# Kernel tuning notes

Hardware: AMD Instinct MI355X
Metric: run time of the kernel (lower is better)

## Reference

```python
import jax, jax.numpy as jnp
import numpy as np

N_NODES = 100000
N_EDGES = 1600000
D_FEAT = 256
HIDDEN = 256
N_CLASSES = 64


def gcn_conv(x, edge_index, W, b, num_nodes):
    """PyG GCNConv: h = W x; add self loops; symmetric D^-1/2 (A+I) D^-1/2 aggregation; + bias."""
    h = x @ W  # [N, out]
    loop = jnp.arange(num_nodes, dtype=edge_index.dtype)
    row = jnp.concatenate([edge_index[0], loop])  # source nodes
    col = jnp.concatenate([edge_index[1], loop])  # target nodes
    deg = jax.ops.segment_sum(jnp.ones_like(col, dtype=h.dtype), col, num_segments=num_nodes)
    dinv = jnp.where(deg > 0, jax.lax.rsqrt(deg), 0.0)
    norm = dinv[row] * dinv[col]  # per-edge normalization
    out = jax.ops.segment_sum(h[row] * norm[:, None], col, num_segments=num_nodes)
    return out + b


def setup_inputs() -> dict:
    key = jax.random.key(0)
    k1, k2, k3, k4 = jax.random.split(key, 4)
    x = jax.random.normal(k1, (N_NODES, D_FEAT), dtype=jnp.float32)
    edge_index = jax.random.randint(k2, (2, N_EDGES), 0, N_NODES, dtype=jnp.int64)
    W1 = jax.random.normal(k3, (D_FEAT, HIDDEN), dtype=jnp.float32) * (1.0 / np.sqrt(D_FEAT))
    b1 = jnp.zeros((HIDDEN,), dtype=jnp.float32)
    W2 = jax.random.normal(k4, (HIDDEN, N_CLASSES), dtype=jnp.float32) * (1.0 / np.sqrt(HIDDEN))
    b2 = jnp.zeros((N_CLASSES,), dtype=jnp.float32)
    return {"x": x, "edge_index": edge_index, "W1": W1, "b1": b1, "W2": W2, "b2": b2}


def reference(x, edge_index, W1, b1, W2, b2):
    # conv1 -> relu -> dropout (eval mode: identity) -> conv2
    h = gcn_conv(x, edge_index, W1, b1, N_NODES)
    h = jax.nn.relu(h)
    out = gcn_conv(h, edge_index, W2, b2, N_NODES)  # [N, num_classes]
    return out
```

## Files before the change

### kernel.cpp

```cpp
#include <hip/hip_runtime.h>
#include <hip/hip_bf16.h>

#define N_NODES 100000
#define N_EDGES 1600000
#define D_FEAT 256
#define HIDDEN 256
#define N_CLASSES 64

#define NBKT 391
#define TILE 4096
#define CAP  8192
#define RB_TOT 6256

typedef __attribute__((ext_vector_type(8))) short bf16x8;
typedef __attribute__((ext_vector_type(4))) float f32x4;

__device__ inline float b2f(ushort u) {
    unsigned v = ((unsigned)u) << 16;
    float f; __builtin_memcpy(&f, &v, 4); return f;
}
__device__ inline ushort f2b(float f) {
    unsigned u; __builtin_memcpy(&u, &f, 4);
    unsigned r = (u + 0x7fffu + ((u >> 16) & 1u)) >> 16;
    return (ushort)r;
}

__global__ __launch_bounds__(256)
void zero_bcnt(int* bcnt) {
    int i = blockIdx.x * 256 + threadIdx.x;
    if (i < NBKT) bcnt[i] = 0;
}

__global__ __launch_bounds__(256)
void bin_count(const int* __restrict__ cols, int* bcnt, int nE) {
    __shared__ int h[NBKT];
    int t = threadIdx.x;
    for (int i = t; i < NBKT; i += 256) h[i] = 0;
    __syncthreads();
    for (long e = (long)blockIdx.x * 256 + t; e < nE; e += (long)gridDim.x * 256)
        atomicAdd(&h[cols[e] >> 8], 1);
    __syncthreads();
    for (int i = t; i < NBKT; i += 256)
        if (h[i]) atomicAdd(&bcnt[i], h[i]);
}

__global__ __launch_bounds__(256)
void bucket_scan(const int* __restrict__ bcnt, int* __restrict__ bbase,
                 int* __restrict__ bcur, int* __restrict__ offsets) {
    __shared__ int sd[256];
    int t = threadIdx.x;
    int i0 = 2 * t, i1 = 2 * t + 1;
    int a = (i0 < NBKT) ? bcnt[i0] : 0;
    int b = (i1 < NBKT) ? bcnt[i1] : 0;
    int s = a + b;
    sd[t] = s; __syncthreads();
    #pragma unroll
    for (int off = 1; off < 256; off <<= 1) {
        int v = (t >= off) ? sd[t - off] : 0;
        __syncthreads();
        sd[t] += v;
        __syncthreads();
    }
    int ex = sd[t] - s;
    if (i0 <= NBKT) bbase[i0] = ex;
    if (i0 < NBKT)  bcur[i0] = ex;
    if (i1 <= NBKT) bbase[i1] = ex + a;
    if (i1 < NBKT)  bcur[i1] = ex + a;
    if (t == 0) offsets[N_NODES] = N_EDGES;
}

__global__ __launch_bounds__(256)
void bin_scatter(const int* __restrict__ rows, const int* __restrict__ cols,
                 int* bcur, unsigned* __restrict__ bins, int nE)
{
    __shared__ unsigned recs[TILE];
    __shared__ ushort bos[TILE];
    __shared__ int hist[NBKT], excl[NBKT], cursor[NBKT], gbase[NBKT];
    __shared__ int sd[256];
    int t = threadIdx.x;
    long e0 = (long)blockIdx.x * TILE;
    int cnt = (int)min((long)TILE, (long)nE - e0);
    for (int i = t; i < NBKT; i += 256) hist[i] = 0;
    __syncthreads();
    int myrow[TILE / 256], mycol[TILE / 256];
    #pragma unroll
    for (int k = 0; k < TILE / 256; ++k) {
        int i = k * 256 + t;
        if (i < cnt) {
            myrow[k] = rows[e0 + i];
            mycol[k] = cols[e0 + i];
            atomicAdd(&hist[mycol[k] >> 8], 1);
        }
    }
    __syncthreads();
    {
        int i0 = 2 * t, i1 = 2 * t + 1;
        int a = (i0 < NBKT) ? hist[i0] : 0;
        int b = (i1 < NBKT) ? hist[i1] : 0;
        int s = a + b;
        sd[t] = s; __syncthreads();
        #pragma unroll
        for (int off = 1; off < 256; off <<= 1) {
            int v = (t >= off) ? sd[t - off] : 0;
            __syncthreads();
            sd[t] += v;
            __syncthreads();
        }
        int ex = sd[t] - s;
        if (i0 < NBKT) { excl[i0] = ex;     cursor[i0] = ex; }
        if (i1 < NBKT) { excl[i1] = ex + a; cursor[i1] = ex + a; }
    }
    __syncthreads();
    #pragma unroll
    for (int k = 0; k < TILE / 256; ++k) {
        int i = k * 256 + t;
        if (i < cnt) {
            int b = mycol[k] >> 8;
            int s = atomicAdd(&cursor[b], 1);
            recs[s] = ((unsigned)(mycol[k] & 255) << 24) | (unsigned)myrow[k];
            bos[s] = (ushort)b;
        }
    }
    __syncthreads();
    for (int i = t; i < NBKT; i += 256)
        if (hist[i] > 0) gbase[i] = atomicAdd(&bcur[i], hist[i]);
    __syncthreads();
    for (int i = t; i < cnt; i += 256) {
        int b = bos[i];
        bins[gbase[b] + (i - excl[b])] = recs[i];
    }
}

__global__ __launch_bounds__(256)
void bucket_fill(const unsigned* __restrict__ bins, const int* __restrict__ bbase,
                 int* __restrict__ offsets, float* __restrict__ dinv,
                 int* __restrict__ esrc)
{
    int b = blockIdx.x, t = threadIdx.x;
    int s0 = bbase[b], s1 = bbase[b + 1];
    int len = s1 - s0;
    __shared__ int cnt[256];
    __shared__ int sd[256];
    __shared__ int cur[256];
    __shared__ int stage[CAP];
    cnt[t] = 0;
    __syncthreads();
    for (int i = t; i < len; i += 256) atomicAdd(&cnt[bins[s0 + i] >> 24], 1);
    __syncthreads();
    int c = cnt[t];
    sd[t] = c; __syncthreads();
    #pragma unroll
    for (int off = 1; off < 256; off <<= 1) {
        int v = (t >= off) ? sd[t - off] : 0;
        __syncthreads();
        sd[t] += v;
        __syncthreads();
    }
    int ex = sd[t] - c;
    cur[t] = ex;
    int node = b * 256 + t;
    if (node < N_NODES) {
        offsets[node] = s0 + ex;
        dinv[node] = rsqrtf(1.0f + (float)c);
    }
    __syncthreads();
    if (len <= CAP) {
        for (int i = t; i < len; i += 256) {
            unsigned r = bins[s0 + i];
            int p = atomicAdd(&cur[r >> 24], 1);
            stage[p] = (int)(r & 0xFFFFFFu);
        }
        __syncthreads();
        for (int i = t; i < len; i += 256) esrc[s0 + i] = stage[i];
    } else {
        for (int i = t; i < len; i += 256) {
            unsigned r = bins[s0 + i];
            int p = atomicAdd(&cur[r >> 24], 1);
            esrc[s0 + p] = (int)(r & 0xFFFFFFu);
        }
    }
}

__global__ __launch_bounds__(256)
void fragw(const float* __restrict__ W1, ushort* __restrict__ wfh,
           ushort* __restrict__ wfl,
           const float* __restrict__ W2, ushort* __restrict__ wf2) {
    int t = blockIdx.x * 256 + threadIdx.x;
    int lane = t & 63;
    int m = lane & 15, quad = lane >> 4;
    if (t < 8192) {
        int ks = t >> 10, nb = (t >> 6) & 15;
        ushort h8[8], l8[8];
        #pragma unroll
        for (int j = 0; j < 8; ++j) {
            int k = ks * 32 + quad * 8 + j;
            float w = W1[k * HIDDEN + nb * 16 + m];
            h8[j] = f2b(w);
            l8[j] = f2b(w - b2f(h8[j]));
        }
        long off = ((long)(ks * 16 + nb) * 64 + lane) * 8;
        *(ushort4*)&wfh[off]     = make_ushort4(h8[0], h8[1], h8[2], h8[3]);
        *(ushort4*)&wfh[off + 4] = make_ushort4(h8[4], h8[5], h8[6], h8[7]);
        *(ushort4*)&wfl[off]     = make_ushort4(l8[0], l8[1], l8[2], l8[3]);
        *(ushort4*)&wfl[off + 4] = make_ushort4(l8[4], l8[5], l8[6], l8[7]);
    } else {
        int u = t - 8192;
        int ks = u >> 8, nb = (u >> 6) & 3;
        ushort h8[8];
        #pragma unroll
        for (int j = 0; j < 8; ++j) {
            int k = ks * 32 + quad * 8 + j;
            h8[j] = f2b(W2[k * N_CLASSES + nb * 16 + m]);
        }
        long off = ((long)(ks * 4 + nb) * 64 + lane) * 8;
        *(ushort4*)&wf2[off]     = make_ushort4(h8[0], h8[1], h8[2], h8[3]);
        *(ushort4*)&wf2[off + 4] = make_ushort4(h8[4], h8[5], h8[6], h8[7]);
    }
}

__global__ __launch_bounds__(256)
void splitx(const float* __restrict__ x, ushort* __restrict__ xh,
            ushort* __restrict__ xl)
{
    int w = blockIdx.x * 4 + (threadIdx.x >> 6);
    int lane = threadIdx.x & 63;
    int rb = w >> 3, ks = w & 7;
    int m = lane & 15, quad = lane >> 4;
    int row = rb * 16 + m;
    float vv[8];
    if (row < N_NODES) {
        const float* p = x + (long)row * D_FEAT + ks * 32 + quad * 8;
        float4 v0 = *(const float4*)p;
        float4 v1 = *(const float4*)(p + 4);
        vv[0] = v0.x; vv[1] = v0.y; vv[2] = v0.z; vv[3] = v0.w;
        vv[4] = v1.x; vv[5] = v1.y; vv[6] = v1.z; vv[7] = v1.w;
    } else {
        #pragma unroll
        for (int j = 0; j < 8; ++j) vv[j] = 0.f;
    }
    ushort h8[8], l8[8];
    #pragma unroll
    for (int j = 0; j < 8; ++j) {
        unsigned u; __builtin_memcpy(&u, &vv[j], 4);
        ushort hh = (ushort)(u >> 16);
        h8[j] = hh;
        l8[j] = f2b(vv[j] - b2f(hh));
    }
    long off = ((long)w * 64 + lane) * 8;
    *(ushort4*)&xh[off]     = make_ushort4(h8[0], h8[1], h8[2], h8[3]);
    *(ushort4*)&xh[off + 4] = make_ushort4(h8[4], h8[5], h8[6], h8[7]);
    *(ushort4*)&xl[off]     = make_ushort4(l8[0], l8[1], l8[2], l8[3]);
    *(ushort4*)&xl[off + 4] = make_ushort4(l8[4], l8[5], l8[6], l8[7]);
}

__global__ __launch_bounds__(256)
void gemm1_mfma(const ushort* __restrict__ xh, const ushort* __restrict__ xl,
                const ushort* __restrict__ wfh, const ushort* __restrict__ wfl,
                const float* __restrict__ dinv, ushort* __restrict__ hs)
{
    int tid = threadIdx.x;
    int lane = tid & 63;
    int wm = (tid >> 6) & 1;
    int wn = tid >> 7;
    int row0 = blockIdx.y * 128 + wm * 64;
    int rb0 = blockIdx.y * 8 + wm * 4;
    int nb0 = blockIdx.x * 8 + wn * 4;
    int m = lane & 15, quad = lane >> 4;

    f32x4 acc[4][4];
    #pragma unroll
    for (int i = 0; i < 4; ++i)
        #pragma unroll
        for (int j = 0; j < 4; ++j) acc[i][j] = (f32x4){0.f, 0.f, 0.f, 0.f};

    for (int ks = 0; ks < 8; ++ks) {
        bf16x8 ah[4], al[4];
        #pragma unroll
        for (int mf = 0; mf < 4; ++mf) {
            long aoff = (((long)(rb0 + mf) * 8 + ks) * 64 + lane) * 8;
            ah[mf] = *(const bf16x8*)(xh + aoff);
            al[mf] = *(const bf16x8*)(xl + aoff);
        }
        #pragma unroll
        for (int nbl = 0; nbl < 4; ++nbl) {
            long boff = ((long)(ks * 16 + nb0 + nbl) * 64 + lane) * 8;
            bf16x8 bh = *(const bf16x8*)(wfh + boff);
            bf16x8 bl = *(const bf16x8*)(wfl + boff);
            #pragma unroll
            for (int mf = 0; mf < 4; ++mf) {
                acc[mf][nbl] = __builtin_amdgcn_mfma_f32_16x16x32_bf16(ah[mf], bh, acc[mf][nbl], 0, 0, 0);
                acc[mf][nbl] = __builtin_amdgcn_mfma_f32_16x16x32_bf16(ah[mf], bl, acc[mf][nbl], 0, 0, 0);
                acc[mf][nbl] = __builtin_amdgcn_mfma_f32_16x16x32_bf16(al[mf], bh, acc[mf][nbl], 0, 0, 0);
            }
        }
    }

    #pragma unroll
    for (int mf = 0; mf < 4; ++mf)
        #pragma unroll
        for (int reg = 0; reg < 4; ++reg) {
            int row = row0 + mf * 16 + quad * 4 + reg;
            if (row < N_NODES) {
                float dv = dinv[row];
                #pragma unroll
                for (int nbl = 0; nbl < 4; ++nbl)
                    hs[(long)row * HIDDEN + (nb0 + nbl) * 16 + m] = f2b(acc[mf][nbl][reg] * dv);
            }
        }
}

__global__ __launch_bounds__(256)
void gemm2_mfma(const ushort* __restrict__ r1s, const ushort* __restrict__ wf,
                ushort* __restrict__ h2)
{
    int tid = threadIdx.x;
    int wv = tid >> 6, lane = tid & 63;
    int row0 = blockIdx.x * 256 + wv * 64;
    int m = lane & 15, quad = lane >> 4;

    f32x4 acc[4][4];
    #pragma unroll
    for (int i = 0; i < 4; ++i)
        #pragma unroll
        for (int j = 0; j < 4; ++j) acc[i][j] = (f32x4){0.f, 0.f, 0.f, 0.f};

    for (int ks = 0; ks < 8; ++ks) {
        bf16x8 a[4];
        #pragma unroll
        for (int mf = 0; mf < 4; ++mf) {
            long r = (long)(row0 + mf * 16 + m);
            a[mf] = *(const bf16x8*)(r1s + r * HIDDEN + ks * 32 + quad * 8);
        }
        #pragma unroll
        for (int nb = 0; nb < 4; ++nb) {
            bf16x8 b = *(const bf16x8*)(wf + ((long)(ks * 4 + nb) * 64 + lane) * 8);
            #pragma unroll
            for (int mf = 0; mf < 4; ++mf)
                acc[mf][nb] = __builtin_amdgcn_mfma_f32_16x16x32_bf16(a[mf], b, acc[mf][nb], 0, 0, 0);
        }
    }

    #pragma unroll
    for (int mf = 0; mf < 4; ++mf)
        #pragma unroll
        for (int reg = 0; reg < 4; ++reg) {
            int row = row0 + mf * 16 + quad * 4 + reg;
            if (row < N_NODES) {
                #pragma unroll
                for (int nb = 0; nb < 4; ++nb)
                    h2[(long)row * N_CLASSES + nb * 16 + m] = f2b(acc[mf][nb][reg]);
            }
        }
}

__global__ __launch_bounds__(256)
void agg256(const ushort* __restrict__ src, const int* __restrict__ offsets,
            const int* __restrict__ esrc, const float* __restrict__ dinv,
            const float* __restrict__ b1, ushort* __restrict__ dst)
{
    int wave = threadIdx.x >> 6, lane = threadIdx.x & 63;
    int v = blockIdx.x * 4 + wave;
    int c = lane << 2;
    ushort4 s = *(const ushort4*)&src[(long)v * 256 + c];
    float a0 = b2f(s.x), a1 = b2f(s.y), a2 = b2f(s.z), a3 = b2f(s.w);
    int e = offsets[v], end = offsets[v + 1];
    for (; e + 8 <= end; e += 8) {
        ushort4 u[8];
        #pragma unroll
        for (int j = 0; j < 8; ++j)
            u[j] = *(const ushort4*)&src[(long)esrc[e + j] * 256 + c];
        #pragma unroll
        for (int j = 0; j < 8; ++j) {
            a0 += b2f(u[j].x); a1 += b2f(u[j].y);
            a2 += b2f(u[j].z); a3 += b2f(u[j].w);
        }
    }
    for (; e < end; ++e) {
        ushort4 u = *(const ushort4*)&src[(long)esrc[e] * 256 + c];
        a0 += b2f(u.x); a1 += b2f(u.y); a2 += b2f(u.z); a3 += b2f(u.w);
    }
    float dv = dinv[v];
    float4 bb = *(const float4*)&b1[c];
    float r0 = dv * fmaxf(fmaf(dv, a0, bb.x), 0.f);
    float r1 = dv * fmaxf(fmaf(dv, a1, bb.y), 0.f);
    float r2 = dv * fmaxf(fmaf(dv, a2, bb.z), 0.f);
    float r3 = dv * fmaxf(fmaf(dv, a3, bb.w), 0.f);
    *(ushort4*)&dst[(long)v * 256 + c] = make_ushort4(f2b(r0), f2b(r1), f2b(r2), f2b(r3));
}

__global__ __launch_bounds__(256)
void agg64b(const ushort* __restrict__ src, const int* __restrict__ offsets,
            const int* __restrict__ esrc, const float* __restrict__ dinv,
            const float* __restrict__ b2, float* __restrict__ out)
{
    int wave = threadIdx.x >> 6, lane = threadIdx.x & 63;
    int v = blockIdx.x * 4 + wave;
    float acc = b2f(src[(long)v * 64 + lane]);
    int e = offsets[v], end = offsets[v + 1];
    for (; e + 8 <= end; e += 8) {
        float a[8];
        #pragma unroll
        for (int j = 0; j < 8; ++j)
            a[j] = b2f(src[(long)esrc[e + j] * 64 + lane]);
        acc += ((a[0] + a[1]) + (a[2] + a[3])) + ((a[4] + a[5]) + (a[6] + a[7]));
    }
    for (; e < end; ++e) acc += b2f(src[(long)esrc[e] * 64 + lane]);
    out[(long)v * 64 + lane] = fmaf(dinv[v], acc, b2[lane]);
}

#define WS_DINV   0UL
#define WS_OFFS   400000UL
#define WS_BCNT   800016UL
#define WS_BBASE  801584UL
#define WS_BCUR   803152UL
#define WS_ESRC   804720UL
#define WS_BINS   7204720UL
#define WS_WF1H   13604720UL
#define WS_WF1L   13735792UL
#define WS_WF2    13866864UL
#define WS_HS1    13899632UL
#define WS_XH     65116016UL
#define WS_XL     116365168UL
#define WS_R1S    WS_XH
#define WS_H2     WS_XL

extern "C" void kernel_launch(void* const* d_in, const int* in_sizes, int n_in,
                              void* d_out, int out_size, void* d_ws, size_t ws_size,
                              hipStream_t stream)
{
    const float* x  = (const float*)d_in[0];
    const int*   ei = (const int*)d_in[1];
    const float* W1 = (const float*)d_in[2];
    const float* b1 = (const float*)d_in[3];
    const float* W2 = (const float*)d_in[4];
    const float* b2 = (const float*)d_in[5];
    float* out = (float*)d_out;

    const int* rows = ei;
    const int* cols = ei + N_EDGES;

    char* ws = (char*)d_ws;
    float*    dinv    = (float*)(ws + WS_DINV);
    int*      offsets = (int*)(ws + WS_OFFS);
    int*      bcnt    = (int*)(ws + WS_BCNT);
    int*      bbase   = (int*)(ws + WS_BBASE);
    int*      bcur    = (int*)(ws + WS_BCUR);
    int*      esrc    = (int*)(ws + WS_ESRC);
    unsigned* bins    = (unsigned*)(ws + WS_BINS);
    ushort*   wf1h    = (ushort*)(ws + WS_WF1H);
    ushort*   wf1l    = (ushort*)(ws + WS_WF1L);
    ushort*   wf2     = (ushort*)(ws + WS_WF2);
    ushort*   hs1     = (ushort*)(ws + WS_HS1);
    ushort*   xh      = (ushort*)(ws + WS_XH);
    ushort*   xl      = (ushort*)(ws + WS_XL);
    ushort*   r1s     = (ushort*)(ws + WS_R1S);
    ushort*   h2      = (ushort*)(ws + WS_H2);

    zero_bcnt<<<2, 256, 0, stream>>>(bcnt);
    bin_count<<<512, 256, 0, stream>>>(cols, bcnt, N_EDGES);
    bucket_scan<<<1, 256, 0, stream>>>(bcnt, bbase, bcur, offsets);
    bin_scatter<<<(N_EDGES + TILE - 1) / TILE, 256, 0, stream>>>(rows, cols, bcur, bins, N_EDGES);
    bucket_fill<<<NBKT, 256, 0, stream>>>(bins, bbase, offsets, dinv, esrc);

    fragw<<<40, 256, 0, stream>>>(W1, wf1h, wf1l, W2, wf2);
    splitx<<<RB_TOT * 8 / 4, 256, 0, stream>>>(x, xh, xl);

    const int agg_grid = N_NODES / 4;

    {
        dim3 g1(2, (N_NODES + 127) / 128);
        gemm1_mfma<<<g1, 256, 0, stream>>>(xh, xl, wf1h, wf1l, dinv, hs1);
    }
    agg256<<<agg_grid, 256, 0, stream>>>(hs1, offsets, esrc, dinv, b1, r1s);

    gemm2_mfma<<<(N_NODES + 255) / 256, 256, 0, stream>>>(r1s, wf2, h2);
    agg64b<<<agg_grid, 256, 0, stream>>>(h2, offsets, esrc, dinv, b2, out);
}
```

Baseline: 550.7 us.

## Store features in column-chunked layout and aggregate per 16-feature chunk

Intermediate feature matrices (hs1, r1s, h2) move from row-major to a chunked layout of 16 contiguous bf16 features per node, with each chunk stored as its own plane of padded node count. The aggregation kernels now get a 2D grid over nodes and feature chunks. Within a wave, 16 edges are processed in parallel with 4 lanes per edge, and a shuffle reduction combines them. The aim is a gather working set per chunk small enough to stay in cache, at the cost of re-reading the edge lists once per chunk and of 32-byte gathers instead of full rows.

```diff
diff --git a/kernel.cpp b/kernel.cpp
--- a/kernel.cpp
+++ b/kernel.cpp
@@ -11,9 +11,11 @@
 #define TILE 4096
 #define CAP  8192
 #define RB_TOT 6256
+#define NPAD 100096
 
 typedef __attribute__((ext_vector_type(8))) short bf16x8;
 typedef __attribute__((ext_vector_type(4))) float f32x4;
+typedef __attribute__((ext_vector_type(4))) ushort u16x4;
 
 __device__ inline float b2f(ushort u) {
     unsigned v = ((unsigned)u) << 16;
@@ -304,7 +306,7 @@
                 float dv = dinv[row];
                 #pragma unroll
                 for (int nbl = 0; nbl < 4; ++nbl)
-                    hs[(long)row * HIDDEN + (nb0 + nbl) * 16 + m] = f2b(acc[mf][nbl][reg] * dv);
+                    hs[((long)(nb0 + nbl) * NPAD + row) * 16 + m] = f2b(acc[mf][nbl][reg] * dv);
             }
         }
 }
@@ -325,11 +327,13 @@
         for (int j = 0; j < 4; ++j) acc[i][j] = (f32x4){0.f, 0.f, 0.f, 0.f};
 
     for (int ks = 0; ks < 8; ++ks) {
+        int ca = 2 * ks + (quad >> 1);
+        int co = (quad & 1) * 8;
         bf16x8 a[4];
         #pragma unroll
         for (int mf = 0; mf < 4; ++mf) {
             long r = (long)(row0 + mf * 16 + m);
-            a[mf] = *(const bf16x8*)(r1s + r * HIDDEN + ks * 32 + quad * 8);
+            a[mf] = *(const bf16x8*)(r1s + ((long)ca * NPAD + r) * 16 + co);
         }
         #pragma unroll
         for (int nb = 0; nb < 4; ++nb) {
@@ -348,64 +352,87 @@
             if (row < N_NODES) {
                 #pragma unroll
                 for (int nb = 0; nb < 4; ++nb)
-                    h2[(long)row * N_CLASSES + nb * 16 + m] = f2b(acc[mf][nb][reg]);
+                    h2[((long)nb * NPAD + row) * 16 + m] = f2b(acc[mf][nb][reg]);
             }
         }
 }
 
 __global__ __launch_bounds__(256)
-void agg256(const ushort* __restrict__ src, const int* __restrict__ offsets,
-            const int* __restrict__ esrc, const float* __restrict__ dinv,
-            const float* __restrict__ b1, ushort* __restrict__ dst)
+void agg256c(const ushort* __restrict__ src,
+             const int* __restrict__ offsets, const int* __restrict__ esrc,
+             const float* __restrict__ dinv, const float* __restrict__ b1,
+             ushort* __restrict__ dst)
 {
     int wave = threadIdx.x >> 6, lane = threadIdx.x & 63;
     int v = blockIdx.x * 4 + wave;
-    int c = lane << 2;
-    ushort4 s = *(const ushort4*)&src[(long)v * 256 + c];
-    float a0 = b2f(s.x), a1 = b2f(s.y), a2 = b2f(s.z), a3 = b2f(s.w);
-    int e = offsets[v], end = offsets[v + 1];
-    for (; e + 8 <= end; e += 8) {
-        ushort4 u[8];
-        #pragma unroll
-        for (int j = 0; j < 8; ++j)
-            u[j] = *(const ushort4*)&src[(long)esrc[e + j] * 256 + c];
-        #pragma unroll
-        for (int j = 0; j < 8; ++j) {
-            a0 += b2f(u[j].x); a1 += b2f(u[j].y);
-            a2 += b2f(u[j].z); a3 += b2f(u[j].w);
-        }
-    }
-    for (; e < end; ++e) {
-        ushort4 u = *(const ushort4*)&src[(long)esrc[e] * 256 + c];
+    int c = blockIdx.y;
+    int es = lane >> 2, fl = lane & 3;
+    const ushort* cb = src + (long)c * NPAD * 16;
+    float a0 = 0.f, a1 = 0.f, a2 = 0.f, a3 = 0.f;
+    int e0 = offsets[v], end = offsets[v + 1];
+    for (int e = e0 + es; e < end; e += 16) {
+        int s = __builtin_nontemporal_load(&esrc[e]);
+        ushort4 u = *(const ushort4*)&cb[(long)s * 16 + fl * 4];
         a0 += b2f(u.x); a1 += b2f(u.y); a2 += b2f(u.z); a3 += b2f(u.w);
     }
-    float dv = dinv[v];
-    float4 bb = *(const float4*)&b1[c];
-    float r0 = dv * fmaxf(fmaf(dv, a0, bb.x), 0.f);
-    float r1 = dv * fmaxf(fmaf(dv, a1, bb.y), 0.f);
-    float r2 = dv * fmaxf(fmaf(dv, a2, bb.z), 0.f);
-    float r3 = dv * fmaxf(fmaf(dv, a3, bb.w), 0.f);
-    *(ushort4*)&dst[(long)v * 256 + c] = make_ushort4(f2b(r0), f2b(r1), f2b(r2), f2b(r3));
-}
-
-__global__ __launch_bounds__(256)
-void agg64b(const ushort* __restrict__ src, const int* __restrict__ offsets,
-            const int* __restrict__ esrc, const float* __restrict__ dinv,
-            const float* __restrict__ b2, float* __restrict__ out)
+    #pragma unroll
+    for (int msk = 4; msk <= 32; msk <<= 1) {
+        a0 += __shfl_xor(a0, msk);
+        a1 += __shfl_xor(a1, msk);
+        a2 += __shfl_xor(a2, msk);
+        a3 += __shfl_xor(a3, msk);
+    }
+    if (lane < 4) {
+        ushort4 s4 = *(const ushort4*)&cb[(long)v * 16 + fl * 4];
+        a0 += b2f(s4.x); a1 += b2f(s4.y); a2 += b2f(s4.z); a3 += b2f(s4.w);
+        float dv = dinv[v];
+        float4 bb = *(const float4*)&b1[c * 16 + fl * 4];
+        u16x4 o;
+        o.x = f2b(dv * fmaxf(fmaf(dv, a0, bb.x), 0.f));
+        o.y = f2b(dv * fmaxf(fmaf(dv, a1, bb.y), 0.f));
+        o.z = f2b(dv * fmaxf(fmaf(dv, a2, bb.z), 0.f));
+        o.w = f2b(dv * fmaxf(fmaf(dv, a3, bb.w), 0.f));
+        __builtin_nontemporal_store(o, (u16x4*)&dst[((long)c * NPAD + v) * 16 + fl * 4]);
+    }
+}
+
+__global__ __launch_bounds__(256)
+void agg64c(const ushort* __restrict__ src,
+            const int* __restrict__ offsets, const int* __restrict__ esrc,
+            const float* __restrict__ dinv, const float* __restrict__ b2,
+            float* __restrict__ out)
 {
     int wave = threadIdx.x >> 6, lane = threadIdx.x & 63;
     int v = blockIdx.x * 4 + wave;
-    float acc = b2f(src[(long)v * 64 + lane]);
-    int e = offsets[v], end = offsets[v + 1];
-    for (; e + 8 <= end; e += 8) {
-        float a[8];
-        #pragma unroll
-        for (int j = 0; j < 8; ++j)
-            a[j] = b2f(src[(long)esrc[e + j] * 64 + lane]);
-        acc += ((a[0] + a[1]) + (a[2] + a[3])) + ((a[4] + a[5]) + (a[6] + a[7]));
-    }
-    for (; e < end; ++e) acc += b2f(src[(long)esrc[e] * 64 + lane]);
-    out[(long)v * 64 + lane] = fmaf(dinv[v], acc, b2[lane]);
+    int c = blockIdx.y;
+    int es = lane >> 2, fl = lane & 3;
+    const ushort* cb = src + (long)c * NPAD * 16;
+    float a0 = 0.f, a1 = 0.f, a2 = 0.f, a3 = 0.f;
+    int e0 = offsets[v], end = offsets[v + 1];
+    for (int e = e0 + es; e < end; e += 16) {
+        int s = __builtin_nontemporal_load(&esrc[e]);
+        ushort4 u = *(const ushort4*)&cb[(long)s * 16 + fl * 4];
+        a0 += b2f(u.x); a1 += b2f(u.y); a2 += b2f(u.z); a3 += b2f(u.w);
+    }
+    #pragma unroll
+    for (int msk = 4; msk <= 32; msk <<= 1) {
+        a0 += __shfl_xor(a0, msk);
+        a1 += __shfl_xor(a1, msk);
+        a2 += __shfl_xor(a2, msk);
+        a3 += __shfl_xor(a3, msk);
+    }
+    if (lane < 4) {
+        ushort4 s4 = *(const ushort4*)&cb[(long)v * 16 + fl * 4];
+        a0 += b2f(s4.x); a1 += b2f(s4.y); a2 += b2f(s4.z); a3 += b2f(s4.w);
+        float dv = dinv[v];
+        float4 bb = *(const float4*)&b2[c * 16 + fl * 4];
+        f32x4 o;
+        o.x = fmaf(dv, a0, bb.x);
+        o.y = fmaf(dv, a1, bb.y);
+        o.z = fmaf(dv, a2, bb.z);
+        o.w = fmaf(dv, a3, bb.w);
+        __builtin_nontemporal_store(o, (f32x4*)&out[(long)v * 64 + c * 16 + fl * 4]);
+    }
 }
 
 #define WS_DINV   0UL
@@ -419,8 +446,8 @@
 #define WS_WF1L   13735792UL
 #define WS_WF2    13866864UL
 #define WS_HS1    13899632UL
-#define WS_XH     65116016UL
-#define WS_XL     116365168UL
+#define WS_XH     65148784UL
+#define WS_XL     116397936UL
 #define WS_R1S    WS_XH
 #define WS_H2     WS_XL
 
@@ -465,14 +492,18 @@
     fragw<<<40, 256, 0, stream>>>(W1, wf1h, wf1l, W2, wf2);
     splitx<<<RB_TOT * 8 / 4, 256, 0, stream>>>(x, xh, xl);
 
-    const int agg_grid = N_NODES / 4;
-
     {
         dim3 g1(2, (N_NODES + 127) / 128);
         gemm1_mfma<<<g1, 256, 0, stream>>>(xh, xl, wf1h, wf1l, dinv, hs1);
     }
-    agg256<<<agg_grid, 256, 0, stream>>>(hs1, offsets, esrc, dinv, b1, r1s);
+    {
+        dim3 ga(N_NODES / 4, 16);
+        agg256c<<<ga, 256, 0, stream>>>(hs1, offsets, esrc, dinv, b1, r1s);
+    }
 
     gemm2_mfma<<<(N_NODES + 255) / 256, 256, 0, stream>>>(r1s, wf2, h2);
-    agg64b<<<agg_grid, 256, 0, stream>>>(h2, offsets, esrc, dinv, b2, out);
-}
+    {
+        dim3 ga(N_NODES / 4, 4);
+        agg64c<<<ga, 256, 0, stream>>>(h2, offsets, esrc, dinv, b2, out);
+    }
+}
```

After: 1.011 ms. 83.6% more time.
